# Kernel optimization log

Measured on AMD Instinct MI355X. Metric: run time of the kernel, lower is better.

Reference implementation:

```python
import jax, jax.numpy as jnp
import numpy as np
import math

B, F, T = 32, 512, 4000
H, DK, DV = 8, 64, 64

def setup_inputs() -> dict:
    key = jax.random.key(0)
    ks = jax.random.split(key, 8)
    x = jax.random.normal(ks[0], (B, F, T), dtype=jnp.float32)
    weights = jax.random.randint(ks[1], (B, T), 0, 2, dtype=jnp.int32)
    # learned params
    q = jax.random.normal(ks[2], (H, DK), dtype=jnp.float32) / math.sqrt(DK)  # (1,H,1,dk) squeezed
    lim_k = 1.0 / math.sqrt(F)
    Wk = jax.random.uniform(ks[3], (H * DK, F), minval=-lim_k, maxval=lim_k, dtype=jnp.float32)
    bk = jax.random.uniform(ks[4], (H * DK,), minval=-lim_k, maxval=lim_k, dtype=jnp.float32)
    Wv = jax.random.uniform(ks[5], (H * DV, F), minval=-lim_k, maxval=lim_k, dtype=jnp.float32)
    bv = jax.random.uniform(ks[6], (H * DV,), minval=-lim_k, maxval=lim_k, dtype=jnp.float32)
    return {"x": x, "weights": weights, "q": q, "Wk": Wk, "bk": bk, "Wv": Wv, "bv": bv}

def reference(x, weights, q, Wk, bk, Wv, bv):
    # x: (B, F, T) -> transpose to (B, T, F) since dim=-1
    xt = jnp.swapaxes(x, 1, 2)                                  # (B,T,F)
    k = (xt @ Wk.T + bk).reshape(B, T, H, DK)                   # (B,T,H,dk)
    v = (xt @ Wv.T + bv).reshape(B, T, H, DV)                   # (B,T,H,dv)
    # scores: q (H,dk) dot k -> (B,H,T), scaled
    scores = jnp.einsum('hd,bthd->bht', q, k) / math.sqrt(DK)
    mask = (weights == 0)[:, None, :]                           # (B,1,T)
    scores = jnp.where(mask, jnp.float32(-1e30), scores)
    attn = jax.nn.softmax(scores, axis=-1)
    attn = jnp.where(mask, 0.0, attn)                           # (B,H,T)
    out = jnp.einsum('bht,bthv->bhv', attn, v)                  # (B,H,dv)
    return out.reshape(B, H * DV)                               # keepdim=False
```

## Files before the change

### kernel.cpp

```cpp
#include <hip/hip_runtime.h>
#include <math.h>

#define BB 32
#define FF 512
#define TT 4000
#define HH 8
#define NCH 16
#define CHT 256
#define TILE 16

__global__ __launch_bounds__(256) void prep_qk(const float* __restrict__ q,
                                               const float* __restrict__ Wk,
                                               const float* __restrict__ bk,
                                               float* __restrict__ qk,
                                               float* __restrict__ qb) {
    int gid = blockIdx.x * 256 + threadIdx.x;
    int h = gid >> 9, f = gid & 511;
    float s = 0.f;
#pragma unroll 8
    for (int d = 0; d < 64; ++d)
        s += q[h * 64 + d] * Wk[(size_t)(h * 64 + d) * FF + f];
    qk[gid] = s * 0.125f;
    if (gid < HH) {
        float sb = 0.f;
        for (int d = 0; d < 64; ++d) sb += q[gid * 64 + d] * bk[gid * 64 + d];
        qb[gid] = sb * 0.125f;
    }
}

__global__ __launch_bounds__(256) void prep_wvt(const float* __restrict__ Wv,
                                                float* __restrict__ WvT) {
    __shared__ float tile[64][65];
    int hv0 = blockIdx.x * 64, f0 = blockIdx.y * 64;
    int tj = threadIdx.x & 63, ti = threadIdx.x >> 6;
#pragma unroll
    for (int r = 0; r < 16; ++r) {
        int i = ti * 16 + r;
        tile[i][tj] = Wv[(size_t)(hv0 + i) * FF + f0 + tj];
    }
    __syncthreads();
#pragma unroll
    for (int r = 0; r < 16; ++r) {
        int i = ti * 16 + r;
        WvT[(size_t)(f0 + i) * FF + hv0 + tj] = tile[tj][i];
    }
}

#define XS_WORDS (2 * FF * TILE)
#define PS_OFF   XS_WORDS
#define AL_OFF   (PS_OFF + HH * TILE)
#define QB_OFF   (AL_OFF + 8)
#define LDS_FLOATS (QB_OFF + 8)

extern __shared__ float smem[];

__global__ __launch_bounds__(512, 4) void k_fused(
    const float* __restrict__ x, const int* __restrict__ wts,
    const float* __restrict__ qkg, const float* __restrict__ qbg,
    float* __restrict__ y_part, float* __restrict__ m_part,
    float* __restrict__ l_part) {
    float* xs  = smem;
    float* ps  = smem + PS_OFF;
    float* al8 = smem + AL_OFF;
    float* qb8 = smem + QB_OFF;

    const int b = blockIdx.y, ch = blockIdx.x;
    const int tid = threadIdx.x;
    const int w = tid >> 6;
    const int l = tid & 63;
    const int t4 = l & 3;
    const int fs = l >> 2;
    const int h = w;
    const int tstart = ch * CHT;
    const int ntile = (ch == NCH - 1) ? 10 : 16;

    if (tid < 8) qb8[tid] = qbg[tid];

    float qkr[32];
#pragma unroll
    for (int j = 0; j < 32; ++j)
        qkr[j] = qkg[h * FF + fs + 16 * j];

    float yacc[8];
#pragma unroll
    for (int i = 0; i < 8; ++i) yacc[i] = 0.f;
    float m_run = -3.0e38f, l_run = 0.f;

    const float* xb = x + (size_t)b * FF * TT;
    const int* wb = wts + (size_t)b * TT;

    const float* xsc = xb + (size_t)fs * TT + tstart + 4 * t4;

#define STAGE(kt, bi, k0, k1)                                                  \
    {                                                                          \
        int t0_ = tstart + (kt) * TILE;                                        \
        _Pragma("unroll")                                                      \
        for (int k = (k0); k < (k1); ++k) {                                    \
            int u = k * 512 + tid;                                             \
            int f_ = u >> 2, sl = u & 3;                                       \
            int t4g = sl ^ ((f_ >> 1) & 3);                                    \
            const float* g = xb + (size_t)f_ * TT + t0_ + 4 * t4g;             \
            float* ldst = xs + (bi) * (FF * TILE) + (k * 512 + w * 64) * 4;    \
            __builtin_amdgcn_global_load_lds(                                  \
                (const __attribute__((address_space(1))) unsigned int*)g,      \
                (__attribute__((address_space(3))) unsigned int*)ldst,         \
                16, 0, 0);                                                     \
        }                                                                      \
    }

    STAGE(0, 0, 0, 4);
    __syncthreads();

    const float qbh = qb8[h];

    for (int kt = 0; kt < ntile; ++kt) {
        int cur = kt & 1, nxt = cur ^ 1;
        if (kt + 1 < ntile) STAGE(kt + 1, nxt, 0, 4);

        int tglob = tstart + kt * TILE + 4 * t4;
        int4 w4 = *(const int4*)(wb + tglob);
        const float* xg = xsc + kt * TILE;
        float4 s4 = make_float4(0.f, 0.f, 0.f, 0.f);
#pragma unroll
        for (int j = 0; j < 32; ++j) {
            float4 xv = *(const float4*)(xg + (size_t)j * (16 * TT));
            float qv = qkr[j];
            s4.x += qv * xv.x;
            s4.y += qv * xv.y;
            s4.z += qv * xv.z;
            s4.w += qv * xv.w;
        }
#pragma unroll
        for (int mk = 4; mk <= 32; mk <<= 1) {
            s4.x += __shfl_xor(s4.x, mk);
            s4.y += __shfl_xor(s4.y, mk);
            s4.z += __shfl_xor(s4.z, mk);
            s4.w += __shfl_xor(s4.w, mk);
        }
        float sm0 = w4.x ? (s4.x + qbh) : -1e30f;
        float sm1 = w4.y ? (s4.y + qbh) : -1e30f;
        float sm2 = w4.z ? (s4.z + qbh) : -1e30f;
        float sm3 = w4.w ? (s4.w + qbh) : -1e30f;
        float tm = fmaxf(fmaxf(sm0, sm1), fmaxf(sm2, sm3));
#pragma unroll
        for (int mk = 1; mk <= 2; mk <<= 1) tm = fmaxf(tm, __shfl_xor(tm, mk));
        float nm = fmaxf(m_run, tm);
        float al = __expf(m_run - nm);
        float e0 = w4.x ? __expf(sm0 - nm) : 0.f;
        float e1 = w4.y ? __expf(sm1 - nm) : 0.f;
        float e2 = w4.z ? __expf(sm2 - nm) : 0.f;
        float e3 = w4.w ? __expf(sm3 - nm) : 0.f;
        float ts = e0 + e1 + e2 + e3;
#pragma unroll
        for (int mk = 1; mk <= 2; mk <<= 1) ts += __shfl_xor(ts, mk);
        l_run = al * l_run + ts;
        m_run = nm;
        if (fs == 0) *(float4*)(ps + h * TILE + 4 * t4) = make_float4(e0, e1, e2, e3);
        if (l == 0) al8[h] = al;

        asm volatile("s_waitcnt lgkmcnt(0)" ::: "memory");
        __builtin_amdgcn_s_barrier();
        __builtin_amdgcn_sched_barrier(0);

#pragma unroll
        for (int hh = 0; hh < 8; ++hh) yacc[hh] *= al8[hh];
        const float* xcur = xs + cur * (FF * TILE);
        const float* xrow = xcur + tid * TILE;
        int fx = (tid >> 1) & 3;
#pragma unroll
        for (int g = 0; g < 4; ++g) {
            float4 xv = *(const float4*)(xrow + 4 * (g ^ fx));
#pragma unroll
            for (int hh = 0; hh < 8; ++hh) {
                float4 e4 = *(const float4*)(ps + hh * TILE + 4 * g);
                yacc[hh] += e4.x * xv.x + e4.y * xv.y + e4.z * xv.z + e4.w * xv.w;
            }
        }
        __syncthreads();
    }

#pragma unroll
    for (int hh = 0; hh < 8; ++hh)
        y_part[(((size_t)b * NCH + ch) * HH + hh) * FF + tid] = yacc[hh];
    if (l == 0) {
        m_part[(b * NCH + ch) * HH + h] = m_run;
        l_part[(b * NCH + ch) * HH + h] = l_run;
    }
}

__global__ __launch_bounds__(256) void k_combine_out(
    const float* __restrict__ y_part, const float* __restrict__ m_part,
    const float* __restrict__ l_part, const float* __restrict__ WvT,
    const float* __restrict__ bv, float* __restrict__ out) {
    __shared__ float ys[4][512];
    __shared__ float wj[4][NCH];
    __shared__ float invL[4], bsc[4];
    int half = blockIdx.x, b = blockIdx.y, tid = threadIdx.x;
    int h0 = half * 4;
    if (tid < 64) {
        int hl = tid >> 4, j = tid & 15;
        float m = m_part[(b * NCH + j) * HH + h0 + hl];
        float lv = l_part[(b * NCH + j) * HH + h0 + hl];
        float M = m;
#pragma unroll
        for (int mk = 1; mk <= 8; mk <<= 1) M = fmaxf(M, __shfl_xor(M, mk, 16));
        float a = __expf(m - M);
        float L = a * lv;
#pragma unroll
        for (int mk = 1; mk <= 8; mk <<= 1) L += __shfl_xor(L, mk, 16);
        wj[hl][j] = a;
        if (j == 0) {
            invL[hl] = (L > 0.f) ? 1.f / L : 0.f;
            bsc[hl] = (L > 0.f) ? 1.f : 0.f;
        }
    }
    __syncthreads();
    for (int i = tid; i < 2048; i += 256) {
        int hl = i >> 9, f = i & 511;
        float s = 0.f;
#pragma unroll
        for (int j = 0; j < NCH; ++j)
            s += wj[hl][j] * y_part[(((size_t)b * NCH + j) * HH + h0 + hl) * FF + f];
        ys[hl][f] = s * invL[hl];
    }
    __syncthreads();
    int hv = half * 256 + tid;
    int hloc = tid >> 6;
    const float* ysr = ys[hloc];
    float acc = 0.f;
#pragma unroll 8
    for (int f = 0; f < FF; ++f)
        acc += ysr[f] * WvT[(size_t)f * FF + hv];
    out[b * 512 + hv] = acc + bv[hv] * bsc[hloc];
}

extern "C" void kernel_launch(void* const* d_in, const int* in_sizes, int n_in,
                              void* d_out, int out_size, void* d_ws, size_t ws_size,
                              hipStream_t stream) {
    const float* x   = (const float*)d_in[0];
    const int*   wts = (const int*)d_in[1];
    const float* q   = (const float*)d_in[2];
    const float* Wk  = (const float*)d_in[3];
    const float* bk  = (const float*)d_in[4];
    const float* Wv  = (const float*)d_in[5];
    const float* bv  = (const float*)d_in[6];
    float* out = (float*)d_out;
    float* ws  = (float*)d_ws;

    float* qk     = ws;
    float* qb     = ws + 4096;
    float* WvT    = ws + 8192;
    float* y_part = ws + 270336;
    float* m_part = ws + 2367488;
    float* l_part = ws + 2371584;

    prep_qk<<<16, 256, 0, stream>>>(q, Wk, bk, qk, qb);
    prep_wvt<<<dim3(8, 8), 256, 0, stream>>>(Wv, WvT);

    size_t lds_bytes = (size_t)LDS_FLOATS * 4;
    (void)hipFuncSetAttribute((const void*)k_fused,
                              hipFuncAttributeMaxDynamicSharedMemorySize,
                              (int)lds_bytes);
    k_fused<<<dim3(NCH, BB), 512, lds_bytes, stream>>>(
        x, wts, qk, qb, y_part, m_part, l_part);

    k_combine_out<<<dim3(2, BB), 256, 0, stream>>>(
        y_part, m_part, l_part, WvT, bv, out);
}
```

Measured before the change: 506.8 us.

## Compute attention scores from LDS tile instead of re-reading x from global

```diff
diff --git a/kernel.cpp b/kernel.cpp
--- a/kernel.cpp
+++ b/kernel.cpp
@@ -50,7 +50,9 @@
 #define PS_OFF   XS_WORDS
 #define AL_OFF   (PS_OFF + HH * TILE)
 #define QB_OFF   (AL_OFF + 8)
-#define LDS_FLOATS (QB_OFF + 8)
+#define PB_OFF   (QB_OFF + 8)
+#define PB_STRIDE 160
+#define LDS_FLOATS (PB_OFF + 8 * PB_STRIDE)
 
 extern __shared__ float smem[];
 
@@ -59,18 +61,19 @@
     const float* __restrict__ qkg, const float* __restrict__ qbg,
     float* __restrict__ y_part, float* __restrict__ m_part,
     float* __restrict__ l_part) {
-    float* xs  = smem;
-    float* ps  = smem + PS_OFF;
-    float* al8 = smem + AL_OFF;
-    float* qb8 = smem + QB_OFF;
+    float* xs   = smem;
+    float* ps   = smem + PS_OFF;
+    float* al8  = smem + AL_OFF;
+    float* qb8  = smem + QB_OFF;
+    float* pbuf = smem + PB_OFF;
 
     const int b = blockIdx.y, ch = blockIdx.x;
     const int tid = threadIdx.x;
     const int w = tid >> 6;
     const int l = tid & 63;
-    const int t4 = l & 3;
-    const int fs = l >> 2;
-    const int h = w;
+    const int tg  = l & 3;
+    const int hl  = (l >> 2) & 7;
+    const int sub = l >> 5;
     const int tstart = ch * CHT;
     const int ntile = (ch == NCH - 1) ? 10 : 16;
 
@@ -79,7 +82,7 @@
     float qkr[32];
 #pragma unroll
     for (int j = 0; j < 32; ++j)
-        qkr[j] = qkg[h * FF + fs + 16 * j];
+        qkr[j] = qkg[hl * FF + (w << 6) + (sub << 5) + j];
 
     float yacc[8];
 #pragma unroll
@@ -88,8 +91,6 @@
 
     const float* xb = x + (size_t)b * FF * TT;
     const int* wb = wts + (size_t)b * TT;
-
-    const float* xsc = xb + (size_t)fs * TT + tstart + 4 * t4;
 
 #define STAGE(kt, bi, k0, k1)                                                  \
     {                                                                          \
@@ -111,31 +112,44 @@
     STAGE(0, 0, 0, 4);
     __syncthreads();
 
-    const float qbh = qb8[h];
+    const float qbh = qb8[w];
 
     for (int kt = 0; kt < ntile; ++kt) {
         int cur = kt & 1, nxt = cur ^ 1;
         if (kt + 1 < ntile) STAGE(kt + 1, nxt, 0, 4);
 
-        int tglob = tstart + kt * TILE + 4 * t4;
+        int tglob = tstart + kt * TILE + 4 * tg;
         int4 w4 = *(const int4*)(wb + tglob);
-        const float* xg = xsc + kt * TILE;
+        const float* xcur = xs + cur * (FF * TILE);
+        const float* xsl = xcur + ((w << 6) + (sub << 5)) * TILE;
+        float4 sa = make_float4(0.f, 0.f, 0.f, 0.f);
+        float4 sb = make_float4(0.f, 0.f, 0.f, 0.f);
+#pragma unroll
+        for (int j = 0; j < 32; j += 2) {
+            int sw = 4 * (tg ^ ((j >> 1) & 3));
+            float4 x0 = *(const float4*)(xsl + 16 * j + sw);
+            float4 x1 = *(const float4*)(xsl + 16 * (j + 1) + sw);
+            float q0 = qkr[j], q1 = qkr[j + 1];
+            sa.x += q0 * x0.x; sa.y += q0 * x0.y; sa.z += q0 * x0.z; sa.w += q0 * x0.w;
+            sb.x += q1 * x1.x; sb.y += q1 * x1.y; sb.z += q1 * x1.z; sb.w += q1 * x1.w;
+        }
+        sa.x += sb.x; sa.y += sb.y; sa.z += sb.z; sa.w += sb.w;
+        sa.x += __shfl_xor(sa.x, 32);
+        sa.y += __shfl_xor(sa.y, 32);
+        sa.z += __shfl_xor(sa.z, 32);
+        sa.w += __shfl_xor(sa.w, 32);
+        if (l < 32)
+            *(float4*)(pbuf + w * PB_STRIDE + hl * 20 + 4 * tg) = sa;
+
+        asm volatile("s_waitcnt lgkmcnt(0)" ::: "memory");
+        __builtin_amdgcn_s_barrier();
+        __builtin_amdgcn_sched_barrier(0);
+
         float4 s4 = make_float4(0.f, 0.f, 0.f, 0.f);
 #pragma unroll
-        for (int j = 0; j < 32; ++j) {
-            float4 xv = *(const float4*)(xg + (size_t)j * (16 * TT));
-            float qv = qkr[j];
-            s4.x += qv * xv.x;
-            s4.y += qv * xv.y;
-            s4.z += qv * xv.z;
-            s4.w += qv * xv.w;
-        }
-#pragma unroll
-        for (int mk = 4; mk <= 32; mk <<= 1) {
-            s4.x += __shfl_xor(s4.x, mk);
-            s4.y += __shfl_xor(s4.y, mk);
-            s4.z += __shfl_xor(s4.z, mk);
-            s4.w += __shfl_xor(s4.w, mk);
+        for (int w2 = 0; w2 < 8; ++w2) {
+            float4 p = *(const float4*)(pbuf + w2 * PB_STRIDE + w * 20 + 4 * tg);
+            s4.x += p.x; s4.y += p.y; s4.z += p.z; s4.w += p.w;
         }
         float sm0 = w4.x ? (s4.x + qbh) : -1e30f;
         float sm1 = w4.y ? (s4.y + qbh) : -1e30f;
@@ -155,8 +169,8 @@
         for (int mk = 1; mk <= 2; mk <<= 1) ts += __shfl_xor(ts, mk);
         l_run = al * l_run + ts;
         m_run = nm;
-        if (fs == 0) *(float4*)(ps + h * TILE + 4 * t4) = make_float4(e0, e1, e2, e3);
-        if (l == 0) al8[h] = al;
+        if (l < 4) *(float4*)(ps + w * TILE + 4 * tg) = make_float4(e0, e1, e2, e3);
+        if (l == 0) al8[w] = al;
 
         asm volatile("s_waitcnt lgkmcnt(0)" ::: "memory");
         __builtin_amdgcn_s_barrier();
@@ -164,7 +178,6 @@
 
 #pragma unroll
         for (int hh = 0; hh < 8; ++hh) yacc[hh] *= al8[hh];
-        const float* xcur = xs + cur * (FF * TILE);
         const float* xrow = xcur + tid * TILE;
         int fx = (tid >> 1) & 3;
 #pragma unroll
@@ -183,8 +196,8 @@
     for (int hh = 0; hh < 8; ++hh)
         y_part[(((size_t)b * NCH + ch) * HH + hh) * FF + tid] = yacc[hh];
     if (l == 0) {
-        m_part[(b * NCH + ch) * HH + h] = m_run;
-        l_part[(b * NCH + ch) * HH + h] = l_run;
+        m_part[(b * NCH + ch) * HH + w] = m_run;
+        l_part[(b * NCH + ch) * HH + w] = l_run;
     }
 }
 
```

Measured after the change: 524.1 us. 3.4% more time.
